# Kernel optimization log

Hardware: AMD Instinct MI355X
Metric: run time of the kernel (lower is better)

Reference implementation:

```python
import jax, jax.numpy as jnp
import numpy as np

N_EMBD = 1024
N_HEAD = 16
HEAD_DIM = N_EMBD // N_HEAD
EPS = 1e-5


def _gelu_tanh(x):
    c = jnp.sqrt(jnp.asarray(2.0 / jnp.pi, x.dtype))
    return 0.5 * x * (1.0 + jnp.tanh(c * (x + 0.044715 * x ** 3)))


def _layernorm(x, scale, shift):
    # torch.var defaults to unbiased (ddof=1) -- replicate exactly
    mean = jnp.mean(x, axis=-1, keepdims=True)
    var = jnp.var(x, axis=-1, keepdims=True, ddof=1)
    return (x - mean) / jnp.sqrt(var + EPS) * scale + shift


def setup_inputs() -> dict:
    key = jax.random.key(0)
    ks = jax.random.split(key, 8)
    d, h = N_EMBD, 4 * N_EMBD
    s = 0.02
    return {
        "x": jax.random.normal(ks[0], (2, 2048, d), jnp.float32),
        "ln1_scale": jnp.ones((d,), jnp.float32),
        "ln1_shift": jnp.zeros((d,), jnp.float32),
        "wq": jax.random.normal(ks[1], (d, d), jnp.float32) * s,
        "wk": jax.random.normal(ks[2], (d, d), jnp.float32) * s,
        "wv": jax.random.normal(ks[3], (d, d), jnp.float32) * s,
        "w_out": jax.random.normal(ks[4], (d, d), jnp.float32) * s,
        "b_out": jnp.zeros((d,), jnp.float32),
        "ln2_scale": jnp.ones((d,), jnp.float32),
        "ln2_shift": jnp.zeros((d,), jnp.float32),
        "w1": jax.random.normal(ks[5], (d, h), jnp.float32) * s,
        "b1": jnp.zeros((h,), jnp.float32),
        "w2": jax.random.normal(ks[6], (h, d), jnp.float32) * s,
        "b2": jnp.zeros((d,), jnp.float32),
    }


def reference(x, ln1_scale, ln1_shift, wq, wk, wv, w_out, b_out,
              ln2_scale, ln2_shift, w1, b1, w2, b2):
    B, S, D = x.shape
    out = _layernorm(x, ln1_scale, ln1_shift)

    # qkv projections (no bias), split heads: [B, H, S, hd]
    q = (out @ wq).reshape(B, S, N_HEAD, HEAD_DIM).transpose(0, 2, 1, 3)
    k = (out @ wk).reshape(B, S, N_HEAD, HEAD_DIM).transpose(0, 2, 1, 3)
    v = (out @ wv).reshape(B, S, N_HEAD, HEAD_DIM).transpose(0, 2, 1, 3)

    scores = jnp.einsum("bhqd,bhkd->bhqk", q, k)
    causal = jnp.triu(jnp.ones((S, S), bool), k=1)
    # original masks BEFORE scaling; -inf / sqrt(d) is still -inf
    scores = jnp.where(causal, -jnp.inf, scores)
    weights = jax.nn.softmax(scores / jnp.sqrt(jnp.asarray(HEAD_DIM, scores.dtype)), axis=-1)
    ctx = jnp.einsum("bhqk,bhkd->bqhd", weights, v).reshape(B, S, D)
    attn_out = ctx @ w_out + b_out

    out = attn_out + x  # dropout is identity (rate 0)
    shortcut = out
    out = _layernorm(out, ln2_scale, ln2_shift)
    out = _gelu_tanh(out @ w1 + b1) @ w2 + b2
    return out + shortcut
```

## Files before the change

kernel.cpp:

```cpp
#include <hip/hip_runtime.h>
#include <stdint.h>
#include <math.h>

using bf16x8 = __attribute__((ext_vector_type(8))) short;
using f32x4  = __attribute__((ext_vector_type(4))) float;

__device__ __forceinline__ uint16_t f2b(float f) {
    union { float f; uint32_t i; } v; v.f = f;
    uint32_t r = v.i + 0x7fffu + ((v.i >> 16) & 1u);
    return (uint16_t)(r >> 16);
}
__device__ __forceinline__ float b2f(uint16_t u) {
    union { uint32_t i; float f; } v; v.i = ((uint32_t)u) << 16; return v.f;
}

typedef const __attribute__((address_space(1))) void gvoid;
typedef __attribute__((address_space(3))) void svoid;

__global__ __launch_bounds__(256) void fill_zero(float* __restrict__ o, int n) {
    int i = (blockIdx.x * 256 + threadIdx.x) * 4;
    if (i < n) *(float4*)(o + i) = make_float4(0.f, 0.f, 0.f, 0.f);
}

__global__ __launch_bounds__(256) void transpose_qkvo(
    const float* __restrict__ wq, const float* __restrict__ wk,
    const float* __restrict__ wv, const float* __restrict__ wo,
    uint16_t* __restrict__ wqkvT, uint16_t* __restrict__ woT)
{
    const int D = 1024;
    int z = blockIdx.z;
    const float* W = (z == 0) ? wq : (z == 1) ? wk : (z == 2) ? wv : wo;
    uint16_t* Wt = (z < 3) ? (wqkvT + (size_t)z * D * D) : woT;
    __shared__ uint16_t t[32][33];
    int n0 = blockIdx.x * 32, k0 = blockIdx.y * 32;
    int tx = threadIdx.x, ty = threadIdx.y;
    #pragma unroll
    for (int i = ty; i < 32; i += 8)
        t[i][tx] = f2b(W[(size_t)(k0 + i) * D + (n0 + tx)]);
    __syncthreads();
    #pragma unroll
    for (int i = ty; i < 32; i += 8)
        Wt[(size_t)(n0 + i) * D + (k0 + tx)] = t[tx][i];
}

__global__ __launch_bounds__(256) void transpose_f2b(
    const float* __restrict__ W, uint16_t* __restrict__ Wt, int K, int N)
{
    __shared__ uint16_t t[32][33];
    int n0 = blockIdx.x * 32, k0 = blockIdx.y * 32;
    int tx = threadIdx.x, ty = threadIdx.y;
    #pragma unroll
    for (int i = ty; i < 32; i += 8)
        t[i][tx] = f2b(W[(size_t)(k0 + i) * N + (n0 + tx)]);
    __syncthreads();
    #pragma unroll
    for (int i = ty; i < 32; i += 8)
        Wt[(size_t)(n0 + i) * K + (k0 + tx)] = t[tx][i];
}

__global__ __launch_bounds__(256) void ln_kernel(
    const float* __restrict__ src, const float* __restrict__ scale,
    const float* __restrict__ shift, uint16_t* __restrict__ out)
{
    const int D = 1024;
    int row = blockIdx.x, t = threadIdx.x;
    float4 f = *((const float4*)(src + (size_t)row * D) + t);
    float v[4] = {f.x, f.y, f.z, f.w};
    float s1 = v[0] + v[1] + v[2] + v[3];
    float s2 = v[0]*v[0] + v[1]*v[1] + v[2]*v[2] + v[3]*v[3];
    #pragma unroll
    for (int off = 32; off; off >>= 1) {
        s1 += __shfl_xor(s1, off);
        s2 += __shfl_xor(s2, off);
    }
    __shared__ float red[2][4];
    __shared__ float stat[2];
    int wid = t >> 6, lane = t & 63;
    if (lane == 0) { red[0][wid] = s1; red[1][wid] = s2; }
    __syncthreads();
    if (t == 0) {
        float S1 = red[0][0] + red[0][1] + red[0][2] + red[0][3];
        float S2 = red[1][0] + red[1][1] + red[1][2] + red[1][3];
        float mean = S1 / (float)D;
        float var  = fmaxf((S2 - mean * S1) / (float)(D - 1), 0.f);
        stat[0] = mean; stat[1] = rsqrtf(var + 1e-5f);
    }
    __syncthreads();
    float mean = stat[0], rstd = stat[1];
    float4 sc = *((const float4*)scale + t);
    float4 sh = *((const float4*)shift + t);
    uint16_t o[4];
    o[0] = f2b((v[0] - mean) * rstd * sc.x + sh.x);
    o[1] = f2b((v[1] - mean) * rstd * sc.y + sh.y);
    o[2] = f2b((v[2] - mean) * rstd * sc.z + sh.z);
    o[3] = f2b((v[3] - mean) * rstd * sc.w + sh.w);
    uint2 st;
    st.x = (uint32_t)o[0] | ((uint32_t)o[1] << 16);
    st.y = (uint32_t)o[2] | ((uint32_t)o[3] << 16);
    *(uint2*)(out + (size_t)row * D + t * 4) = st;
}

__global__ __launch_bounds__(256) void combine2(
    float* __restrict__ dst, const float* __restrict__ part0,
    const float* __restrict__ resid, const float* __restrict__ bias)
{
    const int D = 1024;
    size_t o = (size_t)blockIdx.x * D + threadIdx.x * 4;
    float4 a = *(float4*)(dst + o);
    float4 b = *(const float4*)(part0 + o);
    float4 c = *(const float4*)(resid + o);
    float4 bv = *((const float4*)bias + threadIdx.x);
    a.x += b.x + c.x + bv.x;
    a.y += b.y + c.y + bv.y;
    a.z += b.z + c.z + bv.z;
    a.w += b.w + c.w + bv.w;
    *(float4*)(dst + o) = a;
}

template <int EPI>
__global__ __launch_bounds__(256) void gemm128(
    const uint16_t* __restrict__ A, const uint16_t* __restrict__ Bt,
    const float* __restrict__ bias, const float* __restrict__ resid,
    void* __restrict__ outp, void* __restrict__ out2,
    int M, int N, int K, int lda)
{
    __shared__ __align__(16) uint16_t As[128 * 32];
    __shared__ __align__(16) uint16_t Bs[128 * 32];
    int tid = threadIdx.x;
    int w = tid >> 6, l = tid & 63;
    int quad = l >> 4, ln = l & 15;

    int Nt = gridDim.x, Mt = gridDim.y;
    int L = blockIdx.y * Nt + blockIdx.x;
    const int GROUP = 8;
    int nig = GROUP * Nt;
    int gid = L / nig;
    int fm = gid * GROUP;
    int gsz = min(Mt - fm, GROUP);
    int rem = L - gid * nig;
    int pid_m = fm + rem % gsz;
    int pid_n = rem / gsz;
    int n0 = pid_n * 128, m0 = pid_m * 128;
    int kofs = (EPI == 5) ? blockIdx.z * K : 0;

    int mo = (w & 1) * 64, no = (w >> 1) * 64;

    int srow = l >> 2;
    int scol = (l & 3) * 8;

    f32x4 acc[4][4];
    #pragma unroll
    for (int mi = 0; mi < 4; ++mi)
        #pragma unroll
        for (int ni = 0; ni < 4; ++ni) acc[mi][ni] = (f32x4){0.f, 0.f, 0.f, 0.f};

    for (int k0 = 0; k0 < K; k0 += 32) {
        __syncthreads();
        #pragma unroll
        for (int p = 0; p < 2; ++p) {
            int arow = p * 64 + w * 16 + srow;
            __builtin_amdgcn_global_load_lds(
                (gvoid*)(A + (size_t)(m0 + arow) * lda + kofs + k0 + scol),
                (svoid*)(As + (p * 64 + w * 16) * 32), 16, 0, 0);
            __builtin_amdgcn_global_load_lds(
                (gvoid*)(Bt + (size_t)(n0 + arow) * lda + kofs + k0 + scol),
                (svoid*)(Bs + (p * 64 + w * 16) * 32), 16, 0, 0);
        }
        __syncthreads();

        bf16x8 af[4], bf[4];
        #pragma unroll
        for (int i = 0; i < 4; ++i)
            af[i] = *(const bf16x8*)(As + (mo + i * 16 + ln) * 32 + quad * 8);
        #pragma unroll
        for (int i = 0; i < 4; ++i)
            bf[i] = *(const bf16x8*)(Bs + (no + i * 16 + ln) * 32 + quad * 8);
        #pragma unroll
        for (int mi = 0; mi < 4; ++mi)
            #pragma unroll
            for (int ni = 0; ni < 4; ++ni)
                acc[mi][ni] = __builtin_amdgcn_mfma_f32_16x16x32_bf16(
                    af[mi], bf[ni], acc[mi][ni], 0, 0, 0);
    }

    float* pout = (EPI == 5) ? (blockIdx.z ? (float*)out2 : (float*)outp) : (float*)outp;

    #pragma unroll
    for (int ni = 0; ni < 4; ++ni) {
        int col = n0 + no + ni * 16 + ln;
        if (EPI == 4 && col >= 2048) {
            int hh = (col - 2048) >> 6, d = (col - 2048) & 63;
            #pragma unroll
            for (int mi = 0; mi < 4; ++mi) {
                int tok = m0 + mo + mi * 16 + quad * 4;
                int bat = tok >> 11, s = tok & 2047;
                uint16_t pk[4];
                #pragma unroll
                for (int r = 0; r < 4; ++r) pk[r] = f2b(acc[mi][ni][r]);
                uint2 st;
                st.x = (uint32_t)pk[0] | ((uint32_t)pk[1] << 16);
                st.y = (uint32_t)pk[2] | ((uint32_t)pk[3] << 16);
                *(uint2*)((uint16_t*)out2 +
                          ((size_t)(bat * 16 + hh) * 64 + d) * 2048 + s) = st;
            }
            continue;
        }
        float bv = (EPI == 1 || EPI == 2) ? bias[col] : 0.f;
        #pragma unroll
        for (int mi = 0; mi < 4; ++mi) {
            #pragma unroll
            for (int r = 0; r < 4; ++r) {
                int row = m0 + mo + mi * 16 + quad * 4 + r;
                float vacc = acc[mi][ni][r] + bv;
                if (EPI == 1) {
                    size_t idx = (size_t)row * N + col;
                    ((float*)outp)[idx] = vacc + resid[idx];
                } else if (EPI == 5) {
                    pout[(size_t)row * N + col] = vacc;
                } else if (EPI == 2) {
                    float x = vacc;
                    float u = 0.7978845608028654f * (x + 0.044715f * x * x * x);
                    float g = x / (1.f + __expf(-2.f * u));
                    ((uint16_t*)outp)[(size_t)row * N + col] = f2b(g);
                } else {
                    float vs = (col < 1024) ? vacc * 0.125f : vacc;
                    ((uint16_t*)outp)[(size_t)(col >> 10) * M * 1024 +
                                      (size_t)row * 1024 + (col & 1023)] = f2b(vs);
                }
            }
        }
    }
}

__device__ __forceinline__ void attn_tile(
    const uint16_t* __restrict__ Kl, const uint16_t* __restrict__ Vl,
    uint16_t* __restrict__ Pw,
    bf16x8 qf0, bf16x8 qf1,
    float* l_r, f32x4* o_acc,
    int qw, int kv0, bool diag, int quad, int ln)
{
    const int LW = 72;
    f32x4 sf[4];
    #pragma unroll
    for (int nt2 = 0; nt2 < 4; ++nt2) {
        const uint16_t* kp = Kl + (nt2 * 16 + ln) * LW + quad * 8;
        bf16x8 k0 = *(const bf16x8*)(kp);
        bf16x8 k1 = *(const bf16x8*)(kp + 32);
        f32x4 z = {0.f, 0.f, 0.f, 0.f};
        z = __builtin_amdgcn_mfma_f32_16x16x32_bf16(qf0, k0, z, 0, 0, 0);
        z = __builtin_amdgcn_mfma_f32_16x16x32_bf16(qf1, k1, z, 0, 0, 0);
        sf[nt2] = z;
    }
    #pragma unroll
    for (int r = 0; r < 4; ++r) {
        float ps = 0.f;
        if (diag) {
            int qrow = qw + quad * 4 + r;
            #pragma unroll
            for (int nt2 = 0; nt2 < 4; ++nt2) {
                int kv = kv0 + nt2 * 16 + ln;
                float pv = (kv <= qrow) ? __expf(sf[nt2][r]) : 0.f;
                sf[nt2][r] = pv;
                ps += pv;
            }
        } else {
            #pragma unroll
            for (int nt2 = 0; nt2 < 4; ++nt2) {
                float pv = __expf(sf[nt2][r]);
                sf[nt2][r] = pv;
                ps += pv;
            }
        }
        ps += __shfl_xor(ps, 1);
        ps += __shfl_xor(ps, 2);
        ps += __shfl_xor(ps, 4);
        ps += __shfl_xor(ps, 8);
        l_r[r] += ps;
    }
    #pragma unroll
    for (int nt2 = 0; nt2 < 4; ++nt2) {
        int c = nt2 * 2 + (ln >> 3);
        int off = ln & 7;
        #pragma unroll
        for (int r = 0; r < 4; ++r) {
            int row = quad * 4 + r;
            int p = c ^ (quad ^ ((r << 1) & 7));
            Pw[row * 64 + p * 8 + off] = f2b(sf[nt2][r]);
        }
    }
    int swl = ((ln >> 2) ^ ((ln & 3) << 1)) & 7;
    int g0 = quad ^ swl;
    int g1 = (quad + 4) ^ swl;
    bf16x8 p0 = *(const bf16x8*)(Pw + ln * 64 + g0 * 8);
    bf16x8 p1 = *(const bf16x8*)(Pw + ln * 64 + g1 * 8);
    #pragma unroll
    for (int dt = 0; dt < 4; ++dt) {
        const uint16_t* vp = Vl + (dt * 16 + ln) * LW + quad * 8;
        bf16x8 v0 = *(const bf16x8*)(vp);
        bf16x8 v1 = *(const bf16x8*)(vp + 32);
        o_acc[dt] = __builtin_amdgcn_mfma_f32_16x16x32_bf16(p0, v0, o_acc[dt], 0, 0, 0);
        o_acc[dt] = __builtin_amdgcn_mfma_f32_16x16x32_bf16(p1, v1, o_acc[dt], 0, 0, 0);
    }
}

__global__ __launch_bounds__(256) void attn_flash(
    const uint16_t* __restrict__ Q,
    const uint16_t* __restrict__ K,
    const uint16_t* __restrict__ Vt,
    uint16_t* __restrict__ O,
    int B, int S, int H)
{
    const int D = 1024;
    const int LW = 72;
    __shared__ uint16_t Kl[64 * 72];
    __shared__ uint16_t Vl[64 * 72];
    __shared__ uint16_t Pl[64 * 64];

    int tid = threadIdx.x;
    int w = tid >> 6, l = tid & 63;
    int quad = l >> 4, ln = l & 15;

    int NT = S / 64;
    int qlo = blockIdx.x;
    int qhi = NT - 1 - qlo;
    int h = blockIdx.y, b = blockIdx.z;
    size_t rb = (size_t)b * S;

    int qwl = qlo * 64 + w * 16;
    int qwh = qhi * 64 + w * 16;

    const uint16_t* qpl = Q + (rb + qwl + ln) * D + h * 64 + quad * 8;
    bf16x8 ql0 = *(const bf16x8*)(qpl);
    bf16x8 ql1 = *(const bf16x8*)(qpl + 32);
    const uint16_t* qph = Q + (rb + qwh + ln) * D + h * 64 + quad * 8;
    bf16x8 qh0 = *(const bf16x8*)(qph);
    bf16x8 qh1 = *(const bf16x8*)(qph + 32);

    const uint16_t* Kbase = K + rb * D + h * 64;
    const uint16_t* Vbase = Vt + (size_t)(b * H + h) * 64 * S;
    uint16_t* Pw = Pl + w * 16 * 64;

    float lL[4] = {0.f, 0.f, 0.f, 0.f};
    float lH[4] = {0.f, 0.f, 0.f, 0.f};
    f32x4 oL[4], oH[4];
    #pragma unroll
    for (int dt = 0; dt < 4; ++dt) {
        oL[dt] = (f32x4){0.f, 0.f, 0.f, 0.f};
        oH[dt] = (f32x4){0.f, 0.f, 0.f, 0.f};
    }

    for (int t = 0; t <= qhi; ++t) {
        int kv0 = t * 64;
        __syncthreads();
        #pragma unroll
        for (int p = 0; p < 2; ++p) {
            int idx = p * 256 + tid;
            int row = idx >> 3, c8 = (idx & 7) * 8;
            *(uint4*)(Kl + row * LW + c8) =
                *(const uint4*)(Kbase + (size_t)(kv0 + row) * D + c8);
            *(uint4*)(Vl + row * LW + c8) =
                *(const uint4*)(Vbase + (size_t)row * S + kv0 + c8);
        }
        __syncthreads();

        attn_tile(Kl, Vl, Pw, qh0, qh1, lH, oH, qwh, kv0, t == qhi, quad, ln);
        if (t <= qlo)
            attn_tile(Kl, Vl, Pw, ql0, ql1, lL, oL, qwl, kv0, t == qlo, quad, ln);
    }

    #pragma unroll
    for (int r = 0; r < 4; ++r) {
        float invH = 1.f / lH[r];
        float invL = 1.f / lL[r];
        uint16_t* oph = O + (rb + qwh + quad * 4 + r) * D + h * 64 + ln;
        uint16_t* opl = O + (rb + qwl + quad * 4 + r) * D + h * 64 + ln;
        #pragma unroll
        for (int dt = 0; dt < 4; ++dt) {
            oph[dt * 16] = f2b(oH[dt][r] * invH);
            opl[dt * 16] = f2b(oL[dt][r] * invL);
        }
    }
}

extern "C" void kernel_launch(void* const* d_in, const int* in_sizes, int n_in,
                              void* d_out, int out_size, void* d_ws, size_t ws_size,
                              hipStream_t stream)
{
    (void)in_sizes; (void)n_in;
    const int B = 2, S = 2048, D = 1024, H = 16, F = 4096;
    const int M = B * S;
    const size_t MB = 1u << 20;

    const float* x    = (const float*)d_in[0];
    const float* ln1s = (const float*)d_in[1];
    const float* ln1b = (const float*)d_in[2];
    const float* wq   = (const float*)d_in[3];
    const float* wk   = (const float*)d_in[4];
    const float* wv   = (const float*)d_in[5];
    const float* wo   = (const float*)d_in[6];
    const float* bo   = (const float*)d_in[7];
    const float* ln2s = (const float*)d_in[8];
    const float* ln2b = (const float*)d_in[9];
    const float* w1   = (const float*)d_in[10];
    const float* b1   = (const float*)d_in[11];
    const float* w2   = (const float*)d_in[12];
    const float* b2   = (const float*)d_in[13];

    if (ws_size < 56 * MB) {
        fill_zero<<<(out_size + 1023) / 1024, 256, 0, stream>>>((float*)d_out, out_size);
        return;
    }
    bool full = ws_size >= 72 * MB;

    char* base = (char*)d_ws;
    uint16_t* woT    = (uint16_t*)(base + 0 * MB);
    uint16_t* wqkvT  = (uint16_t*)(base + 2 * MB);
    uint16_t* ln1o   = (uint16_t*)(base + 8 * MB);
    uint16_t* qb     = (uint16_t*)(base + 16 * MB);
    uint16_t* vbT    = (uint16_t*)(base + 32 * MB);
    uint16_t* ctx    = (uint16_t*)(base + 40 * MB);
    uint16_t* kb     = (uint16_t*)(base + 24 * MB);
    uint16_t* w1T    = (uint16_t*)(base + 0 * MB);
    float*    res1   = (float*)   (base + (full ? 56 : 16) * MB);
    uint16_t* ln2o   = (uint16_t*)(base + (full ? 8 : 32) * MB);
    uint16_t* w2T    = (uint16_t*)(base + (full ? 16 : 40) * MB);
    uint16_t* h1     = (uint16_t*)(base + (full ? 24 : 48) * MB);
    float*    part0  = (float*)   (base + 0 * MB);
    float*    partP  = (float*)   (base + 8 * MB);

    dim3 tb(32, 8);
    transpose_qkvo<<<dim3(D / 32, D / 32, 4), tb, 0, stream>>>(
        wq, wk, wv, wo, wqkvT, woT);

    ln_kernel<<<M, 256, 0, stream>>>(x, ln1s, ln1b, ln1o);

    gemm128<4><<<dim3(3072 / 128, M / 128), 256, 0, stream>>>(
        ln1o, wqkvT, nullptr, nullptr, qb, vbT, M, 3072, D, D);

    attn_flash<<<dim3(S / 128, H, B), 256, 0, stream>>>(qb, kb, vbT, ctx, B, S, H);

    if (full) {
        gemm128<5><<<dim3(D / 128, M / 128, 2), 256, 0, stream>>>(
            ctx, woT, nullptr, nullptr, partP, res1, M, D, D / 2, D);
        combine2<<<M, 256, 0, stream>>>(res1, partP, x, bo);
    } else {
        gemm128<1><<<dim3(D / 128, M / 128), 256, 0, stream>>>(
            ctx, woT, bo, x, res1, nullptr, M, D, D, D);
    }

    ln_kernel<<<M, 256, 0, stream>>>(res1, ln2s, ln2b, ln2o);

    transpose_f2b<<<dim3(F / 32, D / 32), tb, 0, stream>>>(w1, w1T, D, F);
    transpose_f2b<<<dim3(D / 32, F / 32), tb, 0, stream>>>(w2, w2T, F, D);

    if (full) {
        gemm128<2><<<dim3(F / 128, M / 128), 256, 0, stream>>>(
            ln2o, w1T, b1, nullptr, h1, nullptr, M, F, D, D);
        gemm128<5><<<dim3(D / 128, M / 128, 2), 256, 0, stream>>>(
            h1, w2T, nullptr, nullptr, part0, d_out, M, D, F / 2, F);
        combine2<<<M, 256, 0, stream>>>((float*)d_out, part0, res1, b2);
    } else {
        const int MH = M / 2;
        for (int half = 0; half < 2; ++half) {
            size_t ro = (size_t)half * MH;
            gemm128<2><<<dim3(F / 128, MH / 128), 256, 0, stream>>>(
                ln2o + ro * D, w1T, b1, nullptr, h1, nullptr, MH, F, D, D);
            gemm128<1><<<dim3(D / 128, MH / 128), 256, 0, stream>>>(
                h1, w2T, b2, res1 + ro * D, (float*)d_out + ro * D, nullptr, MH, D, F, F);
        }
    }
}
```

Measured before the change: 404.8 us.

## Fuse residual combine with LayerNorm2 and double K-step per GEMM barrier

Adds a combine2ln kernel that sums the split-K partials, residual and bias, then computes LayerNorm2 in the same pass and writes the bf16 output. This removes one full read of res1 and one kernel launch. The GEMM main loop now loads two 32-wide K slices into two LDS buffers per iteration, halving the number of __syncthreads pairs. In exchange it doubles LDS use per block, which may lower occupancy, and it assumes K is a multiple of 64.

```diff
diff --git a/kernel.cpp b/kernel.cpp
--- a/kernel.cpp
+++ b/kernel.cpp
@@ -117,6 +117,57 @@
     *(float4*)(dst + o) = a;
 }
 
+__global__ __launch_bounds__(256) void combine2ln(
+    float* __restrict__ res1, const float* __restrict__ part0,
+    const float* __restrict__ x, const float* __restrict__ bo,
+    const float* __restrict__ scale, const float* __restrict__ shift,
+    uint16_t* __restrict__ out)
+{
+    const int D = 1024;
+    int row = blockIdx.x, t = threadIdx.x;
+    size_t o = (size_t)row * D + t * 4;
+    float4 a = *(float4*)(res1 + o);
+    float4 b = *(const float4*)(part0 + o);
+    float4 c = *(const float4*)(x + o);
+    float4 bv = *((const float4*)bo + t);
+    float v[4] = {a.x + b.x + c.x + bv.x, a.y + b.y + c.y + bv.y,
+                  a.z + b.z + c.z + bv.z, a.w + b.w + c.w + bv.w};
+    *(float4*)(res1 + o) = make_float4(v[0], v[1], v[2], v[3]);
+
+    float s1 = v[0] + v[1] + v[2] + v[3];
+    float s2 = v[0]*v[0] + v[1]*v[1] + v[2]*v[2] + v[3]*v[3];
+    #pragma unroll
+    for (int off = 32; off; off >>= 1) {
+        s1 += __shfl_xor(s1, off);
+        s2 += __shfl_xor(s2, off);
+    }
+    __shared__ float red[2][4];
+    __shared__ float stat[2];
+    int wid = t >> 6, lane = t & 63;
+    if (lane == 0) { red[0][wid] = s1; red[1][wid] = s2; }
+    __syncthreads();
+    if (t == 0) {
+        float S1 = red[0][0] + red[0][1] + red[0][2] + red[0][3];
+        float S2 = red[1][0] + red[1][1] + red[1][2] + red[1][3];
+        float mean = S1 / (float)D;
+        float var  = fmaxf((S2 - mean * S1) / (float)(D - 1), 0.f);
+        stat[0] = mean; stat[1] = rsqrtf(var + 1e-5f);
+    }
+    __syncthreads();
+    float mean = stat[0], rstd = stat[1];
+    float4 sc = *((const float4*)scale + t);
+    float4 sh = *((const float4*)shift + t);
+    uint16_t ob[4];
+    ob[0] = f2b((v[0] - mean) * rstd * sc.x + sh.x);
+    ob[1] = f2b((v[1] - mean) * rstd * sc.y + sh.y);
+    ob[2] = f2b((v[2] - mean) * rstd * sc.z + sh.z);
+    ob[3] = f2b((v[3] - mean) * rstd * sc.w + sh.w);
+    uint2 st;
+    st.x = (uint32_t)ob[0] | ((uint32_t)ob[1] << 16);
+    st.y = (uint32_t)ob[2] | ((uint32_t)ob[3] << 16);
+    *(uint2*)(out + (size_t)row * D + t * 4) = st;
+}
+
 template <int EPI>
 __global__ __launch_bounds__(256) void gemm128(
     const uint16_t* __restrict__ A, const uint16_t* __restrict__ Bt,
@@ -124,8 +175,8 @@
     void* __restrict__ outp, void* __restrict__ out2,
     int M, int N, int K, int lda)
 {
-    __shared__ __align__(16) uint16_t As[128 * 32];
-    __shared__ __align__(16) uint16_t Bs[128 * 32];
+    __shared__ __align__(16) uint16_t As[2][128 * 32];
+    __shared__ __align__(16) uint16_t Bs[2][128 * 32];
     int tid = threadIdx.x;
     int w = tid >> 6, l = tid & 63;
     int quad = l >> 4, ln = l & 15;
@@ -154,33 +205,40 @@
         #pragma unroll
         for (int ni = 0; ni < 4; ++ni) acc[mi][ni] = (f32x4){0.f, 0.f, 0.f, 0.f};
 
-    for (int k0 = 0; k0 < K; k0 += 32) {
+    for (int k0 = 0; k0 < K; k0 += 64) {
         __syncthreads();
         #pragma unroll
         for (int p = 0; p < 2; ++p) {
             int arow = p * 64 + w * 16 + srow;
-            __builtin_amdgcn_global_load_lds(
-                (gvoid*)(A + (size_t)(m0 + arow) * lda + kofs + k0 + scol),
-                (svoid*)(As + (p * 64 + w * 16) * 32), 16, 0, 0);
-            __builtin_amdgcn_global_load_lds(
-                (gvoid*)(Bt + (size_t)(n0 + arow) * lda + kofs + k0 + scol),
-                (svoid*)(Bs + (p * 64 + w * 16) * 32), 16, 0, 0);
+            int ldst = (p * 64 + w * 16) * 32;
+            const uint16_t* ga = A  + (size_t)(m0 + arow) * lda + kofs + k0 + scol;
+            const uint16_t* gb = Bt + (size_t)(n0 + arow) * lda + kofs + k0 + scol;
+            #pragma unroll
+            for (int s = 0; s < 2; ++s) {
+                __builtin_amdgcn_global_load_lds(
+                    (gvoid*)(ga + s * 32), (svoid*)(As[s] + ldst), 16, 0, 0);
+                __builtin_amdgcn_global_load_lds(
+                    (gvoid*)(gb + s * 32), (svoid*)(Bs[s] + ldst), 16, 0, 0);
+            }
         }
         __syncthreads();
 
-        bf16x8 af[4], bf[4];
-        #pragma unroll
-        for (int i = 0; i < 4; ++i)
-            af[i] = *(const bf16x8*)(As + (mo + i * 16 + ln) * 32 + quad * 8);
-        #pragma unroll
-        for (int i = 0; i < 4; ++i)
-            bf[i] = *(const bf16x8*)(Bs + (no + i * 16 + ln) * 32 + quad * 8);
-        #pragma unroll
-        for (int mi = 0; mi < 4; ++mi)
-            #pragma unroll
-            for (int ni = 0; ni < 4; ++ni)
-                acc[mi][ni] = __builtin_amdgcn_mfma_f32_16x16x32_bf16(
-                    af[mi], bf[ni], acc[mi][ni], 0, 0, 0);
+        #pragma unroll
+        for (int s = 0; s < 2; ++s) {
+            bf16x8 af[4], bf[4];
+            #pragma unroll
+            for (int i = 0; i < 4; ++i)
+                af[i] = *(const bf16x8*)(As[s] + (mo + i * 16 + ln) * 32 + quad * 8);
+            #pragma unroll
+            for (int i = 0; i < 4; ++i)
+                bf[i] = *(const bf16x8*)(Bs[s] + (no + i * 16 + ln) * 32 + quad * 8);
+            #pragma unroll
+            for (int mi = 0; mi < 4; ++mi)
+                #pragma unroll
+                for (int ni = 0; ni < 4; ++ni)
+                    acc[mi][ni] = __builtin_amdgcn_mfma_f32_16x16x32_bf16(
+                        af[mi], bf[ni], acc[mi][ni], 0, 0, 0);
+        }
     }
 
     float* pout = (EPI == 5) ? (blockIdx.z ? (float*)out2 : (float*)outp) : (float*)outp;
@@ -442,13 +500,12 @@
     if (full) {
         gemm128<5><<<dim3(D / 128, M / 128, 2), 256, 0, stream>>>(
             ctx, woT, nullptr, nullptr, partP, res1, M, D, D / 2, D);
-        combine2<<<M, 256, 0, stream>>>(res1, partP, x, bo);
+        combine2ln<<<M, 256, 0, stream>>>(res1, partP, x, bo, ln2s, ln2b, ln2o);
     } else {
         gemm128<1><<<dim3(D / 128, M / 128), 256, 0, stream>>>(
             ctx, woT, bo, x, res1, nullptr, M, D, D, D);
-    }
-
-    ln_kernel<<<M, 256, 0, stream>>>(res1, ln2s, ln2b, ln2o);
+        ln_kernel<<<M, 256, 0, stream>>>(res1, ln2s, ln2b, ln2o);
+    }
 
     transpose_f2b<<<dim3(F / 32, D / 32), tb, 0, stream>>>(w1, w1T, D, F);
     transpose_f2b<<<dim3(D / 32, F / 32), tb, 0, stream>>>(w2, w2T, F, D);
```

Result: faster. 377.4 us (-6.8%).
